# Kernel tuning notes

Measured on AMD Instinct MI355X. Metric: run time of the kernel, lower is better.

The kernel has to match this reference:

```python
import jax, jax.numpy as jnp
import numpy as np

ATT_DIM = 2048
NUM_HEADS = 16
NUM_KV_GROUPS = 4
HEAD_DIM = 128
CONTEXT_LENGTH = 2048
ROPE_BASE = 10000.0
GROUP_SIZE = NUM_HEADS // NUM_KV_GROUPS
BATCH = 2


def _precompute_rope_sin(context_length, head_dim, rope_base):
    # thetas over rope_dim = head_dim // 2, exponent uses rope_dim (as in source)
    rope_dim = head_dim // 2
    j = jnp.arange(rope_dim, dtype=jnp.float32)
    thetas = 1.0 / rope_base ** (2.0 * j / rope_dim)
    positions = jnp.arange(context_length, dtype=jnp.float32)
    angles = positions[:, None] * thetas[None, :]          # [CD, HD//2]
    angles = jnp.concatenate([angles, angles], axis=-1)    # [CD, HD]
    return jnp.sin(angles)                                  # cos is unused (see bug note)


def _apply_rope(qk, sin):
    # FAITHFUL to source bug: in compute_rope, `cos` is overwritten with the
    # broadcast `sin`, so the returned value is qk*sin + qk_2*sin.
    hd = qk.shape[-1]
    qkr = qk[..., : hd // 2]
    qki = qk[..., hd // 2 :]
    qk2 = jnp.concatenate([-qki, qkr], axis=-1)
    sin_b = sin[None, None, : qk.shape[2], :]
    return qk * sin_b + qk2 * sin  # second term broadcasts full-length sin (requires cd==context_length)


def setup_inputs() -> dict:
    key = jax.random.key(0)
    ks = jax.random.split(key, 6)
    s = 0.02
    x = jax.random.normal(ks[0], (BATCH, CONTEXT_LENGTH, ATT_DIM), dtype=jnp.float32)
    Wq = jax.random.normal(ks[1], (ATT_DIM, HEAD_DIM * NUM_HEADS), dtype=jnp.float32) * s
    Wk = jax.random.normal(ks[2], (ATT_DIM, HEAD_DIM * NUM_KV_GROUPS), dtype=jnp.float32) * s
    Wv = jax.random.normal(ks[3], (ATT_DIM, HEAD_DIM * NUM_KV_GROUPS), dtype=jnp.float32) * s
    Wo = jax.random.normal(ks[4], (HEAD_DIM * NUM_HEADS, HEAD_DIM * NUM_HEADS), dtype=jnp.float32) * s
    bo = jax.random.normal(ks[5], (HEAD_DIM * NUM_HEADS,), dtype=jnp.float32) * s
    return {"x": x, "Wq": Wq, "Wk": Wk, "Wv": Wv, "Wo": Wo, "bo": bo}


def reference(x, Wq, Wk, Wv, Wo, bo):
    bd, cd, ed = x.shape
    sin = _precompute_rope_sin(CONTEXT_LENGTH, HEAD_DIM, ROPE_BASE)

    q = (x @ Wq).reshape(bd, cd, NUM_HEADS, HEAD_DIM).transpose(0, 2, 1, 3)      # [B,NH,CD,HD]
    k = (x @ Wk).reshape(bd, cd, NUM_KV_GROUPS, HEAD_DIM).transpose(0, 2, 1, 3)  # [B,Nkv,CD,HD]
    v = (x @ Wv).reshape(bd, cd, NUM_KV_GROUPS, HEAD_DIM).transpose(0, 2, 1, 3)

    q = _apply_rope(q, sin)
    k = _apply_rope(k, sin)

    k = jnp.repeat(k, GROUP_SIZE, axis=1)  # [B,NH,CD,HD]
    v = jnp.repeat(v, GROUP_SIZE, axis=1)

    a = jnp.einsum("bhqd,bhkd->bhqk", q, k)  # [B,NH,CD,CD]
    causal = jnp.triu(jnp.ones((cd, cd), dtype=bool), k=1)
    a = jnp.where(causal[None, None], -jnp.inf, a)
    a = jax.nn.softmax(a / jnp.sqrt(jnp.float32(HEAD_DIM)), axis=-1)

    y = jnp.einsum("bhqk,bhkd->bhqd", a, v)                # [B,NH,CD,HD]
    y = y.transpose(0, 2, 1, 3).reshape(bd, cd, HEAD_DIM * NUM_HEADS)
    return y @ Wo + bo
```

## Files before the change

### kernel.cpp

```cpp
#include <hip/hip_runtime.h>
#include <hip/hip_bf16.h>
#include <cstdint>
#include <cstddef>

#define BATCH 2
#define CTX 2048
#define EMB 2048
#define NH 16
#define NG 4
#define HD 128
#define NQK (EMB + 2*NG*HD)
#define MROWS (BATCH*CTX)

typedef __bf16 bf16x8 __attribute__((ext_vector_type(8)));
typedef float  f32x4  __attribute__((ext_vector_type(4)));
typedef float  f32x16 __attribute__((ext_vector_type(16)));

__device__ __forceinline__ ushort f2bf(float f) {
    uint32_t u = __float_as_uint(f);
    u += 0x7FFFu + ((u >> 16) & 1u);
    return (ushort)(u >> 16);
}

__device__ __forceinline__ float bf2f(ushort u) {
    return __uint_as_float((uint32_t)u << 16);
}

__device__ __forceinline__ uint32_t packbf(float a, float b) {
    ushort lo = __builtin_bit_cast(ushort, (__bf16)a);
    ushort hi = __builtin_bit_cast(ushort, (__bf16)b);
    return (uint32_t)lo | ((uint32_t)hi << 16);
}

__device__ __forceinline__ bf16x8 mkfrag(uint32_t a, uint32_t b, uint32_t c, uint32_t d) {
    union { uint32_t u[4]; bf16x8 v; } z;
    z.u[0] = a; z.u[1] = b; z.u[2] = c; z.u[3] = d;
    return z.v;
}

__device__ __forceinline__ void gload_lds16(const void* g, void* l) {
    __builtin_amdgcn_global_load_lds((const __attribute__((address_space(1))) void*)g,
                                     (__attribute__((address_space(3))) void*)l, 16, 0, 0);
}

__global__ __launch_bounds__(256) void k_sintab(float* __restrict__ sintab) {
    int t = blockIdx.x * 256 + threadIdx.x;
    int j = t & 63, p = t >> 6;
    float theta = 1.0f / powf(10000.0f, (float)(2 * j) / 64.0f);
    sintab[t] = sinf((float)p * theta);
}

__global__ __launch_bounds__(256) void k_cvt(const float4* __restrict__ src, ushort4* __restrict__ dst) {
    int i = blockIdx.x * 256 + threadIdx.x;
    float4 v = src[i];
    ushort4 o;
    o.x = f2bf(v.x); o.y = f2bf(v.y); o.z = f2bf(v.z); o.w = f2bf(v.w);
    dst[i] = o;
}

__global__ __launch_bounds__(256) void k_transpose_all(const float* __restrict__ Wq, const float* __restrict__ Wk,
                                                       const float* __restrict__ Wv, const float* __restrict__ Wo,
                                                       ushort* __restrict__ Wt, ushort* __restrict__ Wot) {
    __shared__ float tile[32][33];
    int z = blockIdx.z;
    const float* src; ushort* dst; int src_ld, dst_ld, ncols;
    if (z == 0)      { src = Wq; dst = Wt;                              src_ld = EMB;   dst_ld = EMB; ncols = EMB; }
    else if (z == 1) { src = Wk; dst = Wt + (size_t)EMB * EMB;          src_ld = NG*HD; dst_ld = EMB; ncols = NG*HD; }
    else if (z == 2) { src = Wv; dst = Wt + (size_t)(EMB + NG*HD) * EMB; src_ld = NG*HD; dst_ld = EMB; ncols = NG*HD; }
    else             { src = Wo; dst = Wot;                             src_ld = EMB;   dst_ld = EMB; ncols = EMB; }
    int c0 = blockIdx.x * 32, r0 = blockIdx.y * 32;
    if (c0 >= ncols) return;
    int tx = threadIdx.x, ty = threadIdx.y;
    #pragma unroll
    for (int i = 0; i < 4; ++i)
        tile[ty + i*8][tx] = src[(size_t)(r0 + ty + i*8) * src_ld + c0 + tx];
    __syncthreads();
    #pragma unroll
    for (int i = 0; i < 4; ++i)
        dst[(size_t)(c0 + ty + i*8) * dst_ld + r0 + tx] = f2bf(tile[tx][ty + i*8]);
}

#define CLDS_STRIDE 130
__global__ __launch_bounds__(256) void k_gemm_qkv(const ushort* __restrict__ A, const ushort* __restrict__ Bt,
                                                  const float* __restrict__ sintab,
                                                  ushort* __restrict__ Qf, ushort* __restrict__ Kf,
                                                  ushort* __restrict__ Vf, float qscale) {
    __shared__ __align__(16) char smem[33792];
    int tid = threadIdx.x;
    int lane = tid & 63;
    int wave = tid >> 6;
    int wr = wave >> 1, wc = wave & 1;

    int nbx = gridDim.x;
    int id  = blockIdx.y * nbx + blockIdx.x;
    int cpx = (nbx * gridDim.y) >> 3;
    int sid = (id & 7) * cpx + (id >> 3);
    int bx = sid % nbx, by = sid / nbx;
    int m0 = by * 128, n0 = bx * 128;

    int lr = lane & 15, lg = lane >> 4;

    f32x4 acc[4][4] = {};

    int arow = lane >> 2;
    int kpart = (lane & 3) * 8;

    ushort* As = (ushort*)smem;
    ushort* Bs = (ushort*)(smem + 16384);

    int c0s = (wave*2 + 0) * 512, c1s = (wave*2 + 1) * 512;
    const ushort* ga0 = A  + (size_t)(m0 + (wave*2+0)*16 + arow) * EMB + kpart;
    const ushort* ga1 = A  + (size_t)(m0 + (wave*2+1)*16 + arow) * EMB + kpart;
    const ushort* gb0 = Bt + (size_t)(n0 + (wave*2+0)*16 + arow) * EMB + kpart;
    const ushort* gb1 = Bt + (size_t)(n0 + (wave*2+1)*16 + arow) * EMB + kpart;

    auto stage = [&](int koff, int bufoff) {
        gload_lds16(ga0 + koff, &As[bufoff + c0s]);
        gload_lds16(ga1 + koff, &As[bufoff + c1s]);
        gload_lds16(gb0 + koff, &Bs[bufoff + c0s]);
        gload_lds16(gb1 + koff, &Bs[bufoff + c1s]);
    };
    auto compute = [&](int bufoff) {
        bf16x8 af[4], bfr[4];
        #pragma unroll
        for (int mt = 0; mt < 4; ++mt)
            af[mt] = *(const bf16x8*)&As[bufoff + (wr*64 + mt*16 + lr) * 32 + lg * 8];
        #pragma unroll
        for (int nt = 0; nt < 4; ++nt)
            bfr[nt] = *(const bf16x8*)&Bs[bufoff + (wc*64 + nt*16 + lr) * 32 + lg * 8];
        #pragma unroll
        for (int mt = 0; mt < 4; ++mt)
            #pragma unroll
            for (int nt = 0; nt < 4; ++nt)
                acc[mt][nt] = __builtin_amdgcn_mfma_f32_16x16x32_bf16(af[mt], bfr[nt], acc[mt][nt], 0, 0, 0);
    };

    const int nsteps = EMB / 32;
    stage(0, 0);
    __syncthreads();
    for (int t = 0; t + 2 < nsteps; t += 2) {
        stage(32, 4096);
        compute(0);
        __syncthreads();
        stage(64, 0);
        compute(4096);
        __syncthreads();
        ga0 += 64; ga1 += 64; gb0 += 64; gb1 += 64;
    }
    stage(32, 4096);
    compute(0);
    __syncthreads();
    compute(4096);
    __syncthreads();

    ushort* clds = (ushort*)smem;
    #pragma unroll
    for (int mt = 0; mt < 4; ++mt) {
        #pragma unroll
        for (int nt = 0; nt < 4; ++nt) {
            int col = wc*64 + nt*16 + lr;
            int row = wr*64 + mt*16 + lg*4;
            ushort2 p01, p23;
            p01.x = f2bf(acc[mt][nt][0]); p01.y = f2bf(acc[mt][nt][1]);
            p23.x = f2bf(acc[mt][nt][2]); p23.y = f2bf(acc[mt][nt][3]);
            *(ushort2*)&clds[col*CLDS_STRIDE + row]     = p01;
            *(ushort2*)&clds[col*CLDS_STRIDE + row + 2] = p23;
        }
    }
    __syncthreads();

    int xt = bx;
    int b = m0 >> 11;
    int pos0 = m0 & 2047;

    if (xt < 20) {
        int j = tid & 63;
        int rgrp = tid >> 6;
        ushort* dstb;
        float scl;
        if (xt < 16) { dstb = Qf + (size_t)((b*NH + xt) * 64) * 4096;      scl = qscale; }
        else         { dstb = Kf + (size_t)((b*NG + (xt-16)) * 64) * 4096; scl = 1.0f;   }
        #pragma unroll 4
        for (int it = 0; it < 32; ++it) {
            int row = rgrp + it*4;
            int pos = pos0 + row;
            float a  = bf2f(clds[j*CLDS_STRIDE + row]);
            float bb = bf2f(clds[(j+64)*CLDS_STRIDE + row]);
            float sv = sintab[pos*64 + j] * scl;
            size_t idx = (size_t)(pos>>5)*4096 + (size_t)(j>>4)*512 + ((j>>3)&1)*256 + (pos&31)*8 + (j&7);
            dstb[idx]        = f2bf((a - bb) * sv);
            dstb[idx + 2048] = f2bf((bb + a) * sv);
        }
    } else {
        int g = xt - 20;
        int bg = b*NG + g;
        int ln2 = tid & 31, hi2 = (tid >> 5) & 1, dt = tid >> 6;
        int colc = dt*32 + ln2;
        #pragma unroll
        for (int stp = 0; stp < 4; ++stp) {
            #pragma unroll
            for (int ks = 0; ks < 2; ++ks) {
                int rowb = stp*32 + ks*16 + hi2*8;
                union { ushort2 q[4]; bf16x8 v; } z;
                z.q[0] = *(ushort2*)&clds[colc*CLDS_STRIDE + rowb];
                z.q[1] = *(ushort2*)&clds[colc*CLDS_STRIDE + rowb + 2];
                z.q[2] = *(ushort2*)&clds[colc*CLDS_STRIDE + rowb + 4];
                z.q[3] = *(ushort2*)&clds[colc*CLDS_STRIDE + rowb + 6];
                int step_g = (pos0 >> 5) + stp;
                *(bf16x8*)(Vf + ((size_t)(bg*64 + step_g)*8 + dt*2 + ks) * 512 + (tid & 63) * 8) = z.v;
            }
        }
    }
}

__global__ __launch_bounds__(256) void k_gemm_bt(const ushort* __restrict__ A, const ushort* __restrict__ Bt,
                                                 float* __restrict__ C, int M, int N, int K,
                                                 const float* __restrict__ bias) {
    __shared__ __align__(16) ushort As[2][128 * 32];
    __shared__ __align__(16) ushort Bs[2][128 * 32];
    int tid = threadIdx.x;
    int lane = tid & 63;
    int wave = tid >> 6;
    int wr = wave >> 1, wc = wave & 1;

    int nbx = gridDim.x;
    int id  = blockIdx.y * nbx + blockIdx.x;
    int cpx = (nbx * gridDim.y) >> 3;
    int sid = (id & 7) * cpx + (id >> 3);
    int bx = sid % nbx, by = sid / nbx;
    int m0 = by * 128, n0 = bx * 128;

    int lr = lane & 15, lg = lane >> 4;

    f32x4 acc[4][4] = {};

    int arow = lane >> 2;
    int kpart = (lane & 3) * 8;

    int c0s = (wave*2 + 0) * 512, c1s = (wave*2 + 1) * 512;
    const ushort* ga0 = A  + (size_t)(m0 + (wave*2+0)*16 + arow) * K + kpart;
    const ushort* ga1 = A  + (size_t)(m0 + (wave*2+1)*16 + arow) * K + kpart;
    const ushort* gb0 = Bt + (size_t)(n0 + (wave*2+0)*16 + arow) * K + kpart;
    const ushort* gb1 = Bt + (size_t)(n0 + (wave*2+1)*16 + arow) * K + kpart;

    auto stage = [&](int koff, int buf) {
        gload_lds16(ga0 + koff, &As[buf][c0s]);
        gload_lds16(ga1 + koff, &As[buf][c1s]);
        gload_lds16(gb0 + koff, &Bs[buf][c0s]);
        gload_lds16(gb1 + koff, &Bs[buf][c1s]);
    };
    auto compute = [&](int buf) {
        bf16x8 af[4], bfr[4];
        #pragma unroll
        for (int mt = 0; mt < 4; ++mt)
            af[mt] = *(const bf16x8*)&As[buf][(wr*64 + mt*16 + lr) * 32 + lg * 8];
        #pragma unroll
        for (int nt = 0; nt < 4; ++nt)
            bfr[nt] = *(const bf16x8*)&Bs[buf][(wc*64 + nt*16 + lr) * 32 + lg * 8];
        #pragma unroll
        for (int mt = 0; mt < 4; ++mt)
            #pragma unroll
            for (int nt = 0; nt < 4; ++nt)
                acc[mt][nt] = __builtin_amdgcn_mfma_f32_16x16x32_bf16(af[mt], bfr[nt], acc[mt][nt], 0, 0, 0);
    };

    int nsteps = K >> 5;
    stage(0, 0);
    __syncthreads();
    for (int t = 0; t + 2 < nsteps; t += 2) {
        stage(32, 1);
        compute(0);
        __syncthreads();
        stage(64, 0);
        compute(1);
        __syncthreads();
        ga0 += 64; ga1 += 64; gb0 += 64; gb1 += 64;
    }
    stage(32, 1);
    compute(0);
    __syncthreads();
    compute(1);

    #pragma unroll
    for (int mt = 0; mt < 4; ++mt) {
        #pragma unroll
        for (int nt = 0; nt < 4; ++nt) {
            int col = n0 + wc*64 + nt*16 + lr;
            float bv = bias ? bias[col] : 0.0f;
            #pragma unroll
            for (int r = 0; r < 4; ++r) {
                int row = m0 + wr*64 + mt*16 + lg*4 + r;
                C[(size_t)row * N + col] = acc[mt][nt][r] + bv;
            }
        }
    }
}

__global__ __launch_bounds__(512) void k_attn14(const ushort* __restrict__ Qf, const ushort* __restrict__ Kf,
                                                const ushort* __restrict__ Vf, ushort* __restrict__ y) {
    __shared__ __align__(16) char smem[66048];

    int tid  = threadIdx.x;
    int lane = tid & 63;
    int w    = tid >> 6;
    int hh   = w >> 1, ww = w & 1;
    int B  = blockIdx.x;
    int bg = B & 7;
    int t  = 63 - (B >> 3);
    int b = bg >> 2, g = bg & 3, h = g * 4 + hh;
    int ln = lane & 31, hi = lane >> 5;
    int q0 = t * 32;

    const ushort* kf_g = Kf + (size_t)bg * 64 * 4096;
    const ushort* vf_g = Vf + (size_t)bg * 64 * 4096;

    auto stageKV = [&](int r) {
        #pragma unroll
        for (int s2 = 0; s2 < 2; ++s2) {
            gload_lds16(kf_g + r*8192 + s2*4096 + tid*8, smem + 32768 + s2*8192 + tid*16);
            gload_lds16(vf_g + r*8192 + s2*4096 + tid*8, smem + 49152 + s2*8192 + tid*16);
        }
    };

    #pragma unroll
    for (int s = 0; s < 4; ++s) {
        const ushort* qsrc = Qf + ((size_t)((b*NH + g*4 + s) * 64 + t)) * 4096 + tid * 8;
        gload_lds16(qsrc, smem + s*8192 + tid*16);
    }
    stageKV(0);
    __syncthreads();

    const char* qsl = smem + hh*8192  + lane*16;
    const char* ksl = smem + 32768 + ww*8192 + lane*16;
    const char* vsl = smem + 49152 + ww*8192 + lane*16;

    f32x16 od[4] = {};
    float lsum = 0.0f;

    auto step = [&](bool diag) {
        f32x16 st = {};
        #pragma unroll
        for (int s = 0; s < 8; ++s) {
            bf16x8 kf = *(const bf16x8*)(ksl + s * 1024);
            bf16x8 qf = *(const bf16x8*)(qsl + s * 1024);
            st = __builtin_amdgcn_mfma_f32_32x32x16_bf16(kf, qf, st, 0, 0, 0);
        }
        if (diag) {
            #pragma unroll
            for (int r = 0; r < 16; ++r) {
                int kl = (r & 3) + 8*(r >> 2) + 4*hi;
                if (kl > ln) st[r] = -1e30f;
            }
        }
        #pragma unroll
        for (int r = 0; r < 16; ++r) st[r] = exp2f(st[r]);
        float s8[8];
        #pragma unroll
        for (int r = 0; r < 8; ++r) s8[r] = st[r] + st[r+8];
        #pragma unroll
        for (int r = 0; r < 4; ++r) s8[r] = s8[r] + s8[r+4];
        lsum += (s8[0] + s8[1]) + (s8[2] + s8[3]);

        #pragma unroll
        for (int ks = 0; ks < 2; ++ks) {
            uint32_t w0 = packbf(st[8*ks+0], st[8*ks+1]);
            uint32_t w1 = packbf(st[8*ks+2], st[8*ks+3]);
            uint32_t w2 = packbf(st[8*ks+4], st[8*ks+5]);
            uint32_t w3 = packbf(st[8*ks+6], st[8*ks+7]);
            uint32_t sa = hi ? w0 : w2;
            uint32_t sb = hi ? w1 : w3;
            uint32_t ra = (uint32_t)__shfl_xor((int)sa, 32, 64);
            uint32_t rb = (uint32_t)__shfl_xor((int)sb, 32, 64);
            bf16x8 pa = hi ? mkfrag(ra, rb, w2, w3) : mkfrag(w0, w1, ra, rb);
            #pragma unroll
            for (int dt = 0; dt < 4; ++dt) {
                bf16x8 vf = *(const bf16x8*)(vsl + (dt*2 + ks) * 1024);
                od[dt] = __builtin_amdgcn_mfma_f32_32x32x16_bf16(pa, vf, od[dt], 0, 0, 0);
            }
        }
    };

    int rounds = (t >> 1) + 1;
    for (int r = 0; r < rounds; ++r) {
        int tile = 2*r + ww;
        if (tile <= t) step(tile == t);
        __syncthreads();
        if (r + 1 < rounds) {
            stageKV(r + 1);
            __syncthreads();
        }
    }

    lsum += __shfl_xor(lsum, 32, 64);

    float* sOd = (float*)(smem + hh*16512);
    float* sl  = (float*)(smem + hh*16512 + 16384);
    if (ww == 1) {
        #pragma unroll
        for (int r = 0; r < 16; ++r) {
            int ri = (r & 3) + 8*(r >> 2) + 4*hi;
            #pragma unroll
            for (int dt = 0; dt < 4; ++dt) sOd[ri*128 + dt*32 + ln] = od[dt][r];
        }
        if (hi == 0) sl[ln] = lsum;
    }
    __syncthreads();
    if (ww == 0) {
        float inv = 1.0f / (lsum + sl[ln]);
        #pragma unroll
        for (int r = 0; r < 16; ++r) {
            int ri = (r & 3) + 8*(r >> 2) + 4*hi;
            float ivr = __shfl(inv, ri, 64);
            int row = q0 + ri;
            #pragma unroll
            for (int dt = 0; dt < 4; ++dt) {
                float v = (od[dt][r] + sOd[ri*128 + dt*32 + ln]) * ivr;
                y[((size_t)(b*CTX + row)) * (NH*HD) + h*HD + dt*32 + ln] = f2bf(v);
            }
        }
    }
}

#define SIN_OFF   ((size_t)0)
#define XB_OFF    ((size_t)524288)
#define WT_OFF    ((size_t)17301504)
#define WOT_OFF   ((size_t)29884416)
#define QB_OFF    ((size_t)88604672)
#define KB_OFF    ((size_t)105381888)
#define VT_OFF    ((size_t)109576192)
#define YB_OFF    ((size_t)113770496)

extern "C" void kernel_launch(void* const* d_in, const int* in_sizes, int n_in,
                              void* d_out, int out_size, void* d_ws, size_t ws_size,
                              hipStream_t stream) {
    const float* x  = (const float*)d_in[0];
    const float* Wq = (const float*)d_in[1];
    const float* Wk = (const float*)d_in[2];
    const float* Wv = (const float*)d_in[3];
    const float* Wo = (const float*)d_in[4];
    const float* bo = (const float*)d_in[5];
    float* out = (float*)d_out;
    char* ws = (char*)d_ws;

    float*  sintab = (float*)(ws + SIN_OFF);
    ushort* xb     = (ushort*)(ws + XB_OFF);
    ushort* Wt     = (ushort*)(ws + WT_OFF);
    ushort* Wot    = (ushort*)(ws + WOT_OFF);
    ushort* Qf     = (ushort*)(ws + QB_OFF);
    ushort* Kf     = (ushort*)(ws + KB_OFF);
    ushort* Vf     = (ushort*)(ws + VT_OFF);
    ushort* yb     = (ushort*)(ws + YB_OFF);

    const float qscale = 0.08838834764831845f * 1.4426950408889634f;

    k_sintab<<<512, 256, 0, stream>>>(sintab);
    k_cvt<<<(MROWS * EMB / 4) / 256, 256, 0, stream>>>((const float4*)x, (ushort4*)xb);
    k_transpose_all<<<dim3(64, 64, 4), dim3(32, 8), 0, stream>>>(Wq, Wk, Wv, Wo, Wt, Wot);
    k_gemm_qkv<<<dim3(NQK/128, MROWS/128), 256, 0, stream>>>(xb, Wt, sintab, Qf, Kf, Vf, qscale);
    k_attn14<<<512, 512, 0, stream>>>(Qf, Kf, Vf, yb);
    k_gemm_bt<<<dim3(EMB/128, MROWS/128), 256, 0, stream>>>(yb, Wot, out, MROWS, EMB, EMB, bo);
}
```

Before: 207.7 us.

## Merge prep kernels into one launch and remap GEMM tiles per XCD

The sine-table, x-to-bf16 conversion and weight transpose kernels become a single k_prep launch that dispatches on block index, with each conversion thread now handling two float4s. The goal is to cut two kernel launches and the idle gaps between them. Both GEMM kernels also replace their generic tile swizzle with a fixed mapping that gives each XCD four consecutive row tiles, so blocks sharing A rows land on the same L2. The new mapping hardcodes 32 row tiles (MROWS/128), which matches both launches.

Result: slower. 213.9 us (+3.0%).

```diff
diff --git a/kernel.cpp b/kernel.cpp
--- a/kernel.cpp
+++ b/kernel.cpp
@@ -43,41 +43,55 @@
                                      (__attribute__((address_space(3))) void*)l, 16, 0, 0);
 }
 
-__global__ __launch_bounds__(256) void k_sintab(float* __restrict__ sintab) {
-    int t = blockIdx.x * 256 + threadIdx.x;
-    int j = t & 63, p = t >> 6;
-    float theta = 1.0f / powf(10000.0f, (float)(2 * j) / 64.0f);
-    sintab[t] = sinf((float)p * theta);
-}
-
-__global__ __launch_bounds__(256) void k_cvt(const float4* __restrict__ src, ushort4* __restrict__ dst) {
-    int i = blockIdx.x * 256 + threadIdx.x;
-    float4 v = src[i];
-    ushort4 o;
-    o.x = f2bf(v.x); o.y = f2bf(v.y); o.z = f2bf(v.z); o.w = f2bf(v.w);
-    dst[i] = o;
-}
-
-__global__ __launch_bounds__(256) void k_transpose_all(const float* __restrict__ Wq, const float* __restrict__ Wk,
-                                                       const float* __restrict__ Wv, const float* __restrict__ Wo,
-                                                       ushort* __restrict__ Wt, ushort* __restrict__ Wot) {
+#define PREP_SIN 512
+#define PREP_CVT 4096
+__global__ __launch_bounds__(256) void k_prep(const float* __restrict__ x,
+                                              const float* __restrict__ Wq, const float* __restrict__ Wk,
+                                              const float* __restrict__ Wv, const float* __restrict__ Wo,
+                                              float* __restrict__ sintab, ushort* __restrict__ xb,
+                                              ushort* __restrict__ Wt, ushort* __restrict__ Wot) {
+    int B = blockIdx.x;
+    int tid = threadIdx.x;
+    if (B < PREP_SIN) {
+        int t = B * 256 + tid;
+        int j = t & 63, p = t >> 6;
+        float theta = 1.0f / powf(10000.0f, (float)(2 * j) / 64.0f);
+        sintab[t] = sinf((float)p * theta);
+        return;
+    }
+    if (B < PREP_SIN + PREP_CVT) {
+        int i = (B - PREP_SIN) * 256 + tid;
+        const float4* src = (const float4*)x;
+        ushort4* dst = (ushort4*)xb;
+        #pragma unroll
+        for (int k = 0; k < 2; ++k) {
+            float4 v = src[i*2 + k];
+            ushort4 o;
+            o.x = f2bf(v.x); o.y = f2bf(v.y); o.z = f2bf(v.z); o.w = f2bf(v.w);
+            dst[i*2 + k] = o;
+        }
+        return;
+    }
     __shared__ float tile[32][33];
-    int z = blockIdx.z;
-    const float* src; ushort* dst; int src_ld, dst_ld, ncols;
-    if (z == 0)      { src = Wq; dst = Wt;                              src_ld = EMB;   dst_ld = EMB; ncols = EMB; }
-    else if (z == 1) { src = Wk; dst = Wt + (size_t)EMB * EMB;          src_ld = NG*HD; dst_ld = EMB; ncols = NG*HD; }
-    else if (z == 2) { src = Wv; dst = Wt + (size_t)(EMB + NG*HD) * EMB; src_ld = NG*HD; dst_ld = EMB; ncols = NG*HD; }
-    else             { src = Wo; dst = Wot;                             src_ld = EMB;   dst_ld = EMB; ncols = EMB; }
-    int c0 = blockIdx.x * 32, r0 = blockIdx.y * 32;
+    int zz = B - (PREP_SIN + PREP_CVT);
+    int z = zz >> 12;
+    int rem = zz & 4095;
+    int bxx = rem & 63, byy = rem >> 6;
+    const float* src; ushort* dst; int src_ld, ncols;
+    if (z == 0)      { src = Wq; dst = Wt;                               src_ld = EMB;   ncols = EMB; }
+    else if (z == 1) { src = Wk; dst = Wt + (size_t)EMB * EMB;           src_ld = NG*HD; ncols = NG*HD; }
+    else if (z == 2) { src = Wv; dst = Wt + (size_t)(EMB + NG*HD) * EMB; src_ld = NG*HD; ncols = NG*HD; }
+    else             { src = Wo; dst = Wot;                              src_ld = EMB;   ncols = EMB; }
+    int c0 = bxx * 32, r0 = byy * 32;
     if (c0 >= ncols) return;
-    int tx = threadIdx.x, ty = threadIdx.y;
+    int tx = tid & 31, ty = tid >> 5;
     #pragma unroll
     for (int i = 0; i < 4; ++i)
         tile[ty + i*8][tx] = src[(size_t)(r0 + ty + i*8) * src_ld + c0 + tx];
     __syncthreads();
     #pragma unroll
     for (int i = 0; i < 4; ++i)
-        dst[(size_t)(c0 + ty + i*8) * dst_ld + r0 + tx] = f2bf(tile[tx][ty + i*8]);
+        dst[(size_t)(c0 + ty + i*8) * EMB + r0 + tx] = f2bf(tile[tx][ty + i*8]);
 }
 
 #define CLDS_STRIDE 130
@@ -91,11 +105,11 @@
     int wave = tid >> 6;
     int wr = wave >> 1, wc = wave & 1;
 
-    int nbx = gridDim.x;
-    int id  = blockIdx.y * nbx + blockIdx.x;
-    int cpx = (nbx * gridDim.y) >> 3;
-    int sid = (id & 7) * cpx + (id >> 3);
-    int bx = sid % nbx, by = sid / nbx;
+    int id = blockIdx.y * gridDim.x + blockIdx.x;
+    int xcd = id & 7;
+    int within = id >> 3;
+    int by = xcd * 4 + (within & 3);
+    int bx = within >> 2;
     int m0 = by * 128, n0 = bx * 128;
 
     int lr = lane & 15, lg = lane >> 4;
@@ -223,11 +237,11 @@
     int wave = tid >> 6;
     int wr = wave >> 1, wc = wave & 1;
 
-    int nbx = gridDim.x;
-    int id  = blockIdx.y * nbx + blockIdx.x;
-    int cpx = (nbx * gridDim.y) >> 3;
-    int sid = (id & 7) * cpx + (id >> 3);
-    int bx = sid % nbx, by = sid / nbx;
+    int id = blockIdx.y * gridDim.x + blockIdx.x;
+    int xcd = id & 7;
+    int within = id >> 3;
+    int by = xcd * 4 + (within & 3);
+    int bx = within >> 2;
     int m0 = by * 128, n0 = bx * 128;
 
     int lr = lane & 15, lg = lane >> 4;
@@ -299,7 +313,6 @@
 __global__ __launch_bounds__(512) void k_attn14(const ushort* __restrict__ Qf, const ushort* __restrict__ Kf,
                                                 const ushort* __restrict__ Vf, ushort* __restrict__ y) {
     __shared__ __align__(16) char smem[66048];
-
     int tid  = threadIdx.x;
     int lane = tid & 63;
     int w    = tid >> 6;
@@ -453,9 +466,7 @@
 
     const float qscale = 0.08838834764831845f * 1.4426950408889634f;
 
-    k_sintab<<<512, 256, 0, stream>>>(sintab);
-    k_cvt<<<(MROWS * EMB / 4) / 256, 256, 0, stream>>>((const float4*)x, (ushort4*)xb);
-    k_transpose_all<<<dim3(64, 64, 4), dim3(32, 8), 0, stream>>>(Wq, Wk, Wv, Wo, Wt, Wot);
+    k_prep<<<PREP_SIN + PREP_CVT + 4*4096, 256, 0, stream>>>(x, Wq, Wk, Wv, Wo, sintab, xb, Wt, Wot);
     k_gemm_qkv<<<dim3(NQK/128, MROWS/128), 256, 0, stream>>>(xb, Wt, sintab, Qf, Kf, Vf, qscale);
     k_attn14<<<512, 512, 0, stream>>>(Qf, Kf, Vf, yb);
     k_gemm_bt<<<dim3(EMB/128, MROWS/128), 256, 0, stream>>>(yb, Wot, out, MROWS, EMB, EMB, bo);
```
